# Kernel optimization log

Hardware: AMD Instinct MI355X
Metric: run time of the kernel (lower is better)

Reference implementation:

```python
import jax, jax.numpy as jnp
import numpy as np
import math

B, N, C_IN, C_OUT, K, RATIO = 16, 4096, 256, 512, 16, 0.25
N_OUT = math.ceil(N * RATIO)  # 1024
BN_EPS = 1e-5


def fps_indices(p, n):
    """Farthest point sampling. p: [B,N,3] -> local indices [B,n] (deterministic start at 0, eval mode)."""
    def fps_one(pts):  # [N,3]
        d0 = jnp.sum((pts - pts[0]) ** 2, axis=-1)          # [N]
        idxs0 = jnp.zeros((n,), jnp.int32)                  # idx[0] = 0
        def body(i, st):
            d, idxs = st
            nxt = jnp.argmax(d).astype(jnp.int32)
            idxs = idxs.at[i].set(nxt)
            d = jnp.minimum(d, jnp.sum((pts - pts[nxt]) ** 2, axis=-1))
            return (d, idxs)
        _, idxs = jax.lax.fori_loop(1, n, body, (d0, idxs0))
        return idxs
    return jax.vmap(fps_one)(p)


def setup_inputs() -> dict:
    key = jax.random.key(0)
    ks = jax.random.split(key, 6)
    x = jax.random.normal(ks[0], (B, N, C_IN), jnp.float32)
    p = jax.random.normal(ks[1], (B, N, 3), jnp.float32)
    sid_euc = jax.random.randint(ks[2], (B * N, K), 0, B * N).astype(jnp.int64)
    tid_euc = jax.random.randint(ks[3], (B * N, K), 0, B * N).astype(jnp.int64)
    W = jax.random.normal(ks[4], (C_OUT, C_IN), jnp.float32) * (1.0 / np.sqrt(C_IN))
    b = jax.random.normal(ks[5], (C_OUT,), jnp.float32) * 0.02
    gamma = jnp.ones((C_OUT,), jnp.float32)
    beta = jnp.zeros((C_OUT,), jnp.float32)
    run_mean = jnp.zeros((C_OUT,), jnp.float32)
    run_var = jnp.ones((C_OUT,), jnp.float32)
    return {"x": x, "p": p, "sid_euc": sid_euc, "tid_euc": tid_euc,
            "W": W, "b": b, "gamma": gamma, "beta": beta,
            "run_mean": run_mean, "run_var": run_var}


def reference(x, p, sid_euc, tid_euc, W, b, gamma, beta, run_mean, run_var):
    Bsz, Npts, _ = x.shape
    n = N_OUT
    Kn = sid_euc.shape[1]
    # MLP: pointwise Linear + BatchNorm (eval) + ReLU
    h = jnp.einsum('bnc,oc->bno', x, W) + b                       # [B,N,C_OUT]
    h = (h - run_mean) * (gamma / jnp.sqrt(run_var + BN_EPS)) + beta
    h = jax.nn.relu(h)
    # FPS -> global flat indices into B*N
    fid_local = fps_indices(p, n)                                  # [B,n]
    fid = (fid_local + jnp.arange(Bsz, dtype=jnp.int32)[:, None] * Npts).reshape(-1)
    # sample coords
    p_flat = p.reshape(Bsz * Npts, -1)
    p_out = p_flat[fid].reshape(Bsz, n, -1)                        # [B,n,3]
    # gather K neighbors of each sampled point, max-pool over K
    sid = sid_euc[fid].reshape(-1)                                 # [B*n*K]
    h_flat = h.reshape(Bsz * Npts, -1)
    x_out = h_flat[sid].reshape(Bsz, n, Kn, -1).max(axis=-2)       # [B,n,C_OUT]
    return (x_out, p_out)
```

## Files before the change

### kernel.cpp

```cpp
#include <hip/hip_runtime.h>
#include <hip/hip_bf16.h>

#define BATCH   16
#define NPTS    4096
#define CIN     256
#define COUT    512
#define KNN     16
#define NOUT    1024
#define XOUT_ELEMS 8388608
#define LDA     40

typedef __attribute__((ext_vector_type(4))) float f32x4;
typedef __attribute__((ext_vector_type(8))) short bf16x8;

__device__ __forceinline__ unsigned short f2bf_rne(float f) {
    unsigned u = __float_as_uint(f);
    return (unsigned short)((u + 0x7FFFu + ((u >> 16) & 1u)) >> 16);
}
__device__ __forceinline__ float bf2f(unsigned short s) {
    return __uint_as_float(((unsigned)s) << 16);
}

__device__ __forceinline__ float wave_max_dpp(float v) {
    int x, y;
    x = __float_as_int(v);
    y = __builtin_amdgcn_update_dpp(x, x, 0x111, 0xf, 0xf, false);
    v = fmaxf(v, __int_as_float(y)); x = __float_as_int(v);
    y = __builtin_amdgcn_update_dpp(x, x, 0x112, 0xf, 0xf, false);
    v = fmaxf(v, __int_as_float(y)); x = __float_as_int(v);
    y = __builtin_amdgcn_update_dpp(x, x, 0x114, 0xf, 0xf, false);
    v = fmaxf(v, __int_as_float(y)); x = __float_as_int(v);
    y = __builtin_amdgcn_update_dpp(x, x, 0x118, 0xf, 0xf, false);
    v = fmaxf(v, __int_as_float(y)); x = __float_as_int(v);
    y = __builtin_amdgcn_update_dpp(x, x, 0x142, 0xf, 0xf, false);
    v = fmaxf(v, __int_as_float(y)); x = __float_as_int(v);
    y = __builtin_amdgcn_update_dpp(x, x, 0x143, 0xf, 0xf, false);
    v = fmaxf(v, __int_as_float(y));
    return v;
}

extern "C" __global__ void __launch_bounds__(256)
fused_fps_gemm(const float* __restrict__ x, const float* __restrict__ p,
               const float* __restrict__ W, const float* __restrict__ bias,
               const float* __restrict__ gamma, const float* __restrict__ beta,
               const float* __restrict__ rmean, const float* __restrict__ rvar,
               int* __restrict__ fid, unsigned short* __restrict__ h)
{
    extern __shared__ char smem[];
    const int t = threadIdx.x;

    if (blockIdx.x < BATCH) {
        const int b = blockIdx.x;
        float* lx = (float*)smem;
        float* ly = lx + NPTS;
        float* lz = ly + NPTS;
        unsigned long long* warr = (unsigned long long*)(lz + NPTS);

        const float* pb = p + (size_t)b * NPTS * 3;
        for (int l = t; l < NPTS * 3; l += 256) {
            float v = pb[l];
            int pi = l / 3;
            int c = l - pi * 3;
            if (c == 0) lx[pi] = v; else if (c == 1) ly[pi] = v; else lz[pi] = v;
        }
        __syncthreads();

        float px[16], py[16], pz[16], d[16];
        const int base = t << 4;
#pragma unroll
        for (int j = 0; j < 16; ++j) {
            px[j] = lx[base + j]; py[j] = ly[base + j]; pz[j] = lz[base + j];
            d[j] = 3.4028235e38f;
        }
        if (t == 0) fid[b * NOUT] = b * NPTS;

        int winner = 0;
        for (int i = 1; i < NOUT; ++i) {
            float wx = lx[winner], wy = ly[winner], wz = lz[winner];
            float bestd = -1.0f;
            int   bestj = 0;
#pragma unroll
            for (int j = 0; j < 16; ++j) {
                float dx = __fsub_rn(px[j], wx);
                float dy = __fsub_rn(py[j], wy);
                float dz = __fsub_rn(pz[j], wz);
                float s  = __fadd_rn(__fadd_rn(__fmul_rn(dx, dx), __fmul_rn(dy, dy)),
                                     __fmul_rn(dz, dz));
                float nd = fminf(d[j], s);
                d[j] = nd;
                bool gt = nd > bestd;
                bestd = gt ? nd : bestd;
                bestj = gt ? j  : bestj;
            }
            float vmax = wave_max_dpp(bestd);
            float wmax = __int_as_float(
                __builtin_amdgcn_readlane(__float_as_int(vmax), 63));
            unsigned long long msk = __ballot(bestd == wmax);
            int lead = (int)__builtin_ctzll(msk);
            int wbpi = __builtin_amdgcn_readlane(base + bestj, lead);
            unsigned long long key = ((unsigned long long)__float_as_uint(wmax) << 32)
                                   | (unsigned)(NPTS - 1 - wbpi);
            unsigned long long* wrow = warr + ((i & 1) << 2);
            if ((t & 63) == 0) wrow[t >> 6] = key;
            __syncthreads();
            unsigned long long k0 = wrow[0], k1 = wrow[1], k2 = wrow[2], k3 = wrow[3];
            if (k1 > k0) k0 = k1;
            if (k3 > k2) k2 = k3;
            if (k2 > k0) k0 = k2;
            winner = NPTS - 1 - (int)(unsigned)(k0 & 0xffffffffull);
            if (t == 0) fid[b * NOUT + i] = b * NPTS + winner;
        }
    } else {
        const int bid = blockIdx.x - BATCH;
        const int bm = bid >> 2;
        const int bn = bid & 3;
        short* As = (short*)smem;
        short* Bs = As + 128 * LDA;

        const int lane = t & 63;
        const int wv = t >> 6;
        const int wm = wv >> 1, wn = wv & 1;
        const int quad = lane >> 4, l16 = lane & 15;
        const int m0 = bm * 128, n0 = bn * 128;

        f32x4 acc[4][4];
        const f32x4 zero = {0.0f, 0.0f, 0.0f, 0.0f};
#pragma unroll
        for (int a = 0; a < 4; ++a)
#pragma unroll
            for (int bb = 0; bb < 4; ++bb) acc[a][bb] = zero;

        const int srow = t >> 3;
        const int scol = (t & 7) << 2;

        for (int ks = 0; ks < 8; ++ks) {
            const int k0 = ks * 32;
            __syncthreads();
#pragma unroll
            for (int it = 0; it < 4; ++it) {
                int row = srow + it * 32;
                float4 va = *(const float4*)(x + (size_t)(m0 + row) * CIN + k0 + scol);
                short4 pa = make_short4((short)f2bf_rne(va.x), (short)f2bf_rne(va.y),
                                        (short)f2bf_rne(va.z), (short)f2bf_rne(va.w));
                *(short4*)(As + row * LDA + scol) = pa;
                float4 vb = *(const float4*)(W + (size_t)(n0 + row) * CIN + k0 + scol);
                short4 pb2 = make_short4((short)f2bf_rne(vb.x), (short)f2bf_rne(vb.y),
                                         (short)f2bf_rne(vb.z), (short)f2bf_rne(vb.w));
                *(short4*)(Bs + row * LDA + scol) = pb2;
            }
            __syncthreads();
            bf16x8 af[4], bfr[4];
#pragma unroll
            for (int tm = 0; tm < 4; ++tm)
                af[tm] = *(const bf16x8*)(As + (wm * 64 + tm * 16 + l16) * LDA + quad * 8);
#pragma unroll
            for (int tn = 0; tn < 4; ++tn)
                bfr[tn] = *(const bf16x8*)(Bs + (wn * 64 + tn * 16 + l16) * LDA + quad * 8);
#pragma unroll
            for (int tm = 0; tm < 4; ++tm)
#pragma unroll
                for (int tn = 0; tn < 4; ++tn)
                    acc[tm][tn] = __builtin_amdgcn_mfma_f32_16x16x32_bf16(
                        af[tm], bfr[tn], acc[tm][tn], 0, 0, 0);
        }
#pragma unroll
        for (int tn = 0; tn < 4; ++tn) {
            int c = n0 + wn * 64 + tn * 16 + l16;
            float sc = gamma[c] / sqrtf(rvar[c] + 1e-5f);
            float sh = (bias[c] - rmean[c]) * sc + beta[c];
#pragma unroll
            for (int tm = 0; tm < 4; ++tm) {
                int rbase = m0 + wm * 64 + tm * 16 + quad * 4;
#pragma unroll
                for (int r = 0; r < 4; ++r) {
                    float v = fmaxf(acc[tm][tn][r] * sc + sh, 0.0f);
                    h[(size_t)(rbase + r) * COUT + c] = f2bf_rne(v);
                }
            }
        }
    }
}

extern "C" __global__ void __launch_bounds__(128)
gather_maxpool(const int* __restrict__ sid32, const float* __restrict__ p,
               const int* __restrict__ fid, const unsigned short* __restrict__ h,
               float* __restrict__ out)
{
    const int j = blockIdx.x;
    const int t = threadIdx.x;
    __shared__ int rows[KNN];
    const int frow = fid[j];
    bool is64 = (sid32[1] == 0) && (sid32[3] == 0) && (sid32[5] == 0);
    if (t < KNN) {
        long long e = (long long)frow * KNN + t;
        rows[t] = is64 ? sid32[e * 2] : sid32[e];
    }
    if (t < 3) out[(size_t)XOUT_ELEMS + (size_t)j * 3 + t] = p[(size_t)frow * 3 + t];
    __syncthreads();

    const int c4 = t << 2;
    float m0 = -3.4028235e38f, m1 = m0, m2 = m0, m3 = m0;
#pragma unroll
    for (int k = 0; k < KNN; ++k) {
        const ushort4 v = *(const ushort4*)(h + (size_t)rows[k] * COUT + c4);
        m0 = fmaxf(m0, bf2f(v.x));
        m1 = fmaxf(m1, bf2f(v.y));
        m2 = fmaxf(m2, bf2f(v.z));
        m3 = fmaxf(m3, bf2f(v.w));
    }
    *(float4*)(out + (size_t)j * COUT + c4) = make_float4(m0, m1, m2, m3);
}

extern "C" void kernel_launch(void* const* d_in, const int* in_sizes, int n_in,
                              void* d_out, int out_size, void* d_ws, size_t ws_size,
                              hipStream_t stream)
{
    const float* x     = (const float*)d_in[0];
    const float* p     = (const float*)d_in[1];
    const int*   sid   = (const int*)d_in[2];
    const float* W     = (const float*)d_in[4];
    const float* bias  = (const float*)d_in[5];
    const float* gamma = (const float*)d_in[6];
    const float* beta  = (const float*)d_in[7];
    const float* rmean = (const float*)d_in[8];
    const float* rvar  = (const float*)d_in[9];
    float* out = (float*)d_out;

    int* fid = (int*)d_ws;
    unsigned short* h = (unsigned short*)((char*)d_ws + 65536);

    const size_t lds = 3 * NPTS * 4 + 2 * 4 * 8;
    hipLaunchKernelGGL(fused_fps_gemm, dim3(BATCH + 512 * 4), dim3(256), lds, stream,
                       x, p, W, bias, gamma, beta, rmean, rvar, fid, h);
    hipLaunchKernelGGL(gather_maxpool, dim3(BATCH * NOUT), dim3(128), 0, stream,
                       sid, p, fid, h, out);
}
```

Measured before the change: 745.7 us.

## Fuse gather-maxpool into persistent kernel with flag-based FPS streaming

Merges the gather/maxpool stage into the FPS+GEMM kernel. Gather blocks spin on a GEMM completion counter and on per-sample fid entries, which are pre-filled with -1 by a memset, so gathering can overlap the serial FPS loop instead of waiting for a second launch. The FPS blocks now write sampled coordinates directly, and the inner distance loop uses packed float2 math. The cost is spin-waiting gather blocks that hold CU slots, two extra memsets, and a risk of deadlock or ordering problems if the FPS blocks are not scheduled ahead of the waiting blocks.

```diff
diff --git a/kernel.cpp b/kernel.cpp
--- a/kernel.cpp
+++ b/kernel.cpp
@@ -9,8 +9,11 @@
 #define NOUT    1024
 #define XOUT_ELEMS 8388608
 #define LDA     40
+#define GEMM_BLOCKS 2048
+#define GATHER_BLOCKS 8192
 
 typedef __attribute__((ext_vector_type(4))) float f32x4;
+typedef __attribute__((ext_vector_type(2))) float f32x2;
 typedef __attribute__((ext_vector_type(8))) short bf16x8;
 
 __device__ __forceinline__ unsigned short f2bf_rne(float f) {
@@ -40,21 +43,25 @@
 }
 
 extern "C" __global__ void __launch_bounds__(256)
-fused_fps_gemm(const float* __restrict__ x, const float* __restrict__ p,
-               const float* __restrict__ W, const float* __restrict__ bias,
-               const float* __restrict__ gamma, const float* __restrict__ beta,
-               const float* __restrict__ rmean, const float* __restrict__ rvar,
-               int* __restrict__ fid, unsigned short* __restrict__ h)
+fused_all(const float* __restrict__ x, const float* __restrict__ p,
+          const int* __restrict__ sid32, const float* __restrict__ W,
+          const float* __restrict__ bias, const float* __restrict__ gamma,
+          const float* __restrict__ beta, const float* __restrict__ rmean,
+          const float* __restrict__ rvar, int* __restrict__ fid,
+          unsigned* __restrict__ cnt, unsigned short* __restrict__ h,
+          float* __restrict__ out)
 {
     extern __shared__ char smem[];
     const int t = threadIdx.x;
 
     if (blockIdx.x < BATCH) {
+#pragma clang fp contract(off)
         const int b = blockIdx.x;
         float* lx = (float*)smem;
         float* ly = lx + NPTS;
         float* lz = ly + NPTS;
         unsigned long long* warr = (unsigned long long*)(lz + NPTS);
+        float* pout = out + XOUT_ELEMS + (size_t)b * NOUT * 3;
 
         const float* pb = p + (size_t)b * NPTS * 3;
         for (int l = t; l < NPTS * 3; l += 256) {
@@ -65,32 +72,45 @@
         }
         __syncthreads();
 
-        float px[16], py[16], pz[16], d[16];
+        f32x2 px2[8], py2[8], pz2[8], d2[8];
         const int base = t << 4;
 #pragma unroll
-        for (int j = 0; j < 16; ++j) {
-            px[j] = lx[base + j]; py[j] = ly[base + j]; pz[j] = lz[base + j];
-            d[j] = 3.4028235e38f;
-        }
-        if (t == 0) fid[b * NOUT] = b * NPTS;
+        for (int j = 0; j < 8; ++j) {
+            px2[j] = *(const f32x2*)(lx + base + (j << 1));
+            py2[j] = *(const f32x2*)(ly + base + (j << 1));
+            pz2[j] = *(const f32x2*)(lz + base + (j << 1));
+            d2[j]  = (f32x2){3.4028235e38f, 3.4028235e38f};
+        }
+        if (t == 0)
+            __hip_atomic_store(&fid[b * NOUT], b * NPTS, __ATOMIC_RELAXED,
+                               __HIP_MEMORY_SCOPE_AGENT);
 
         int winner = 0;
         for (int i = 1; i < NOUT; ++i) {
             float wx = lx[winner], wy = ly[winner], wz = lz[winner];
+            if (t == 0) {
+                float* po = pout + (size_t)(i - 1) * 3;
+                po[0] = wx; po[1] = wy; po[2] = wz;
+            }
+            f32x2 wx2 = {wx, wx}, wy2 = {wy, wy}, wz2 = {wz, wz};
             float bestd = -1.0f;
             int   bestj = 0;
 #pragma unroll
-            for (int j = 0; j < 16; ++j) {
-                float dx = __fsub_rn(px[j], wx);
-                float dy = __fsub_rn(py[j], wy);
-                float dz = __fsub_rn(pz[j], wz);
-                float s  = __fadd_rn(__fadd_rn(__fmul_rn(dx, dx), __fmul_rn(dy, dy)),
-                                     __fmul_rn(dz, dz));
-                float nd = fminf(d[j], s);
-                d[j] = nd;
-                bool gt = nd > bestd;
-                bestd = gt ? nd : bestd;
-                bestj = gt ? j  : bestj;
+            for (int j = 0; j < 8; ++j) {
+                f32x2 dx = px2[j] - wx2;
+                f32x2 dy = py2[j] - wy2;
+                f32x2 dz = pz2[j] - wz2;
+                f32x2 s  = ((dx * dx) + (dy * dy)) + (dz * dz);
+                f32x2 nd;
+                nd.x = fminf(d2[j].x, s.x);
+                nd.y = fminf(d2[j].y, s.y);
+                d2[j] = nd;
+                bool g0 = nd.x > bestd;
+                bestd = g0 ? nd.x : bestd;
+                bestj = g0 ? (j << 1) : bestj;
+                bool g1 = nd.y > bestd;
+                bestd = g1 ? nd.y : bestd;
+                bestj = g1 ? (j << 1) + 1 : bestj;
             }
             float vmax = wave_max_dpp(bestd);
             float wmax = __int_as_float(
@@ -108,9 +128,15 @@
             if (k3 > k2) k2 = k3;
             if (k2 > k0) k0 = k2;
             winner = NPTS - 1 - (int)(unsigned)(k0 & 0xffffffffull);
-            if (t == 0) fid[b * NOUT + i] = b * NPTS + winner;
-        }
-    } else {
+            if (t == 0)
+                __hip_atomic_store(&fid[b * NOUT + i], b * NPTS + winner,
+                                   __ATOMIC_RELAXED, __HIP_MEMORY_SCOPE_AGENT);
+        }
+        if (t == 0) {
+            float* po = pout + (size_t)(NOUT - 1) * 3;
+            po[0] = lx[winner]; po[1] = ly[winner]; po[2] = lz[winner];
+        }
+    } else if (blockIdx.x < BATCH + GEMM_BLOCKS) {
         const int bid = blockIdx.x - BATCH;
         const int bm = bid >> 2;
         const int bn = bid & 3;
@@ -178,37 +204,61 @@
                 }
             }
         }
+        __threadfence();
+        __syncthreads();
+        if (t == 0)
+            __hip_atomic_fetch_add(cnt, 1u, __ATOMIC_RELEASE,
+                                   __HIP_MEMORY_SCOPE_AGENT);
+    } else {
+        const int gb = blockIdx.x - (BATCH + GEMM_BLOCKS);
+        const int j0 = gb << 1;
+        int* rows  = (int*)smem;
+        int* frows = rows + 32;
+        const int g = t >> 7, tl = t & 127;
+
+        if (tl == 0) {
+            if (g == 0) {
+                long guard = 0;
+                unsigned c;
+                do {
+                    c = __hip_atomic_load(cnt, __ATOMIC_ACQUIRE,
+                                          __HIP_MEMORY_SCOPE_AGENT);
+                    if (c >= (unsigned)GEMM_BLOCKS) break;
+                    __builtin_amdgcn_s_sleep(32);
+                } while (++guard < (1 << 21));
+            }
+            long guard = 0;
+            int v;
+            do {
+                v = __hip_atomic_load(&fid[j0 + g], __ATOMIC_RELAXED,
+                                      __HIP_MEMORY_SCOPE_AGENT);
+                if (v >= 0) break;
+                __builtin_amdgcn_s_sleep(16);
+            } while (++guard < (1 << 21));
+            frows[g] = v;
+            __threadfence();
+        }
+        __syncthreads();
+        const int frow = frows[g];
+        bool is64 = (sid32[1] == 0) && (sid32[3] == 0) && (sid32[5] == 0);
+        if (tl < KNN) {
+            long long e = (long long)frow * KNN + tl;
+            rows[g * KNN + tl] = is64 ? sid32[e * 2] : sid32[e];
+        }
+        __syncthreads();
+
+        const int c4 = tl << 2;
+        float m0 = -3.4028235e38f, m1 = m0, m2 = m0, m3 = m0;
+#pragma unroll
+        for (int k = 0; k < KNN; ++k) {
+            const ushort4 v = *(const ushort4*)(h + (size_t)rows[g * KNN + k] * COUT + c4);
+            m0 = fmaxf(m0, bf2f(v.x));
+            m1 = fmaxf(m1, bf2f(v.y));
+            m2 = fmaxf(m2, bf2f(v.z));
+            m3 = fmaxf(m3, bf2f(v.w));
+        }
+        *(float4*)(out + (size_t)(j0 + g) * COUT + c4) = make_float4(m0, m1, m2, m3);
     }
-}
-
-extern "C" __global__ void __launch_bounds__(128)
-gather_maxpool(const int* __restrict__ sid32, const float* __restrict__ p,
-               const int* __restrict__ fid, const unsigned short* __restrict__ h,
-               float* __restrict__ out)
-{
-    const int j = blockIdx.x;
-    const int t = threadIdx.x;
-    __shared__ int rows[KNN];
-    const int frow = fid[j];
-    bool is64 = (sid32[1] == 0) && (sid32[3] == 0) && (sid32[5] == 0);
-    if (t < KNN) {
-        long long e = (long long)frow * KNN + t;
-        rows[t] = is64 ? sid32[e * 2] : sid32[e];
-    }
-    if (t < 3) out[(size_t)XOUT_ELEMS + (size_t)j * 3 + t] = p[(size_t)frow * 3 + t];
-    __syncthreads();
-
-    const int c4 = t << 2;
-    float m0 = -3.4028235e38f, m1 = m0, m2 = m0, m3 = m0;
-#pragma unroll
-    for (int k = 0; k < KNN; ++k) {
-        const ushort4 v = *(const ushort4*)(h + (size_t)rows[k] * COUT + c4);
-        m0 = fmaxf(m0, bf2f(v.x));
-        m1 = fmaxf(m1, bf2f(v.y));
-        m2 = fmaxf(m2, bf2f(v.z));
-        m3 = fmaxf(m3, bf2f(v.w));
-    }
-    *(float4*)(out + (size_t)j * COUT + c4) = make_float4(m0, m1, m2, m3);
 }
 
 extern "C" void kernel_launch(void* const* d_in, const int* in_sizes, int n_in,
@@ -226,12 +276,16 @@
     const float* rvar  = (const float*)d_in[9];
     float* out = (float*)d_out;
 
-    int* fid = (int*)d_ws;
-    unsigned short* h = (unsigned short*)((char*)d_ws + 65536);
+    int*      fid = (int*)d_ws;
+    unsigned* cnt = (unsigned*)((char*)d_ws + 65536);
+    unsigned short* h = (unsigned short*)((char*)d_ws + 65792);
+
+    hipMemsetAsync(d_ws, 0xFF, 65536, stream);
+    hipMemsetAsync((char*)d_ws + 65536, 0, 4, stream);
 
     const size_t lds = 3 * NPTS * 4 + 2 * 4 * 8;
-    hipLaunchKernelGGL(fused_fps_gemm, dim3(BATCH + 512 * 4), dim3(256), lds, stream,
-                       x, p, W, bias, gamma, beta, rmean, rvar, fid, h);
-    hipLaunchKernelGGL(gather_maxpool, dim3(BATCH * NOUT), dim3(128), 0, stream,
-                       sid, p, fid, h, out);
-}
+    hipLaunchKernelGGL(fused_all, dim3(BATCH + GEMM_BLOCKS + GATHER_BLOCKS),
+                       dim3(256), lds, stream,
+                       x, p, sid, W, bias, gamma, beta, rmean, rvar,
+                       fid, cnt, h, out);
+}
```

Result: slower. 1.207 ms (+61.9%).

## Widen FPS blocks to 1024 threads and restructure GEMM blocks into dual groups

Applied to the files above, without the earlier changes.

The FPS blocks now use 1024 threads, each owning 4 points instead of 16. This shortens the serial per-iteration distance/argmax work, and the 16 wave keys are reduced with a 64-bit DPP max across lanes. FPS also writes the sampled coordinates directly, so the gather kernel no longer has to. The GEMM blocks become 1024-thread blocks split into two independent 512-thread groups, each computing two 128x128 tiles in sequence. The block-wide syncs are shared by both groups, and the larger block size may lower occupancy.

```diff
diff --git a/kernel.cpp b/kernel.cpp
--- a/kernel.cpp
+++ b/kernel.cpp
@@ -9,8 +9,10 @@
 #define NOUT    1024
 #define XOUT_ELEMS 8388608
 #define LDA     40
+#define DYN_LDS 49408
 
 typedef __attribute__((ext_vector_type(4))) float f32x4;
+typedef __attribute__((ext_vector_type(2))) float f32x2;
 typedef __attribute__((ext_vector_type(8))) short bf16x8;
 
 __device__ __forceinline__ unsigned short f2bf_rne(float f) {
@@ -39,25 +41,41 @@
     return v;
 }
 
-extern "C" __global__ void __launch_bounds__(256)
-fused_fps_gemm(const float* __restrict__ x, const float* __restrict__ p,
-               const float* __restrict__ W, const float* __restrict__ bias,
-               const float* __restrict__ gamma, const float* __restrict__ beta,
-               const float* __restrict__ rmean, const float* __restrict__ rvar,
-               int* __restrict__ fid, unsigned short* __restrict__ h)
+template <int CTRL>
+__device__ __forceinline__ void dpp_u64_max_step(unsigned& klo, unsigned& khi) {
+    unsigned olo = (unsigned)__builtin_amdgcn_update_dpp(
+        (int)klo, (int)klo, CTRL, 0xf, 0xf, false);
+    unsigned ohi = (unsigned)__builtin_amdgcn_update_dpp(
+        (int)khi, (int)khi, CTRL, 0xf, 0xf, false);
+    bool take = (ohi > khi) || (ohi == khi && olo > klo);
+    klo = take ? olo : klo;
+    khi = take ? ohi : khi;
+}
+
+extern "C" __global__ void __launch_bounds__(1024)
+fps_gemm(const float* __restrict__ x, const float* __restrict__ p,
+         const float* __restrict__ W, const float* __restrict__ bias,
+         const float* __restrict__ gamma, const float* __restrict__ beta,
+         const float* __restrict__ rmean, const float* __restrict__ rvar,
+         int* __restrict__ fid, unsigned short* __restrict__ h,
+         float* __restrict__ out)
 {
     extern __shared__ char smem[];
     const int t = threadIdx.x;
+    const int lane = t & 63;
+    const int wv = t >> 6;
 
     if (blockIdx.x < BATCH) {
+#pragma clang fp contract(off)
         const int b = blockIdx.x;
         float* lx = (float*)smem;
         float* ly = lx + NPTS;
         float* lz = ly + NPTS;
         unsigned long long* warr = (unsigned long long*)(lz + NPTS);
+        float* pout = out + XOUT_ELEMS + (size_t)b * NOUT * 3;
 
         const float* pb = p + (size_t)b * NPTS * 3;
-        for (int l = t; l < NPTS * 3; l += 256) {
+        for (int l = t; l < NPTS * 3; l += 1024) {
             float v = pb[l];
             int pi = l / 3;
             int c = l - pi * 3;
@@ -65,32 +83,43 @@
         }
         __syncthreads();
 
-        float px[16], py[16], pz[16], d[16];
-        const int base = t << 4;
-#pragma unroll
-        for (int j = 0; j < 16; ++j) {
-            px[j] = lx[base + j]; py[j] = ly[base + j]; pz[j] = lz[base + j];
-            d[j] = 3.4028235e38f;
+        f32x2 px2[2], py2[2], pz2[2], d2[2];
+        const int base = t << 2;
+#pragma unroll
+        for (int j = 0; j < 2; ++j) {
+            px2[j] = *(const f32x2*)(lx + base + (j << 1));
+            py2[j] = *(const f32x2*)(ly + base + (j << 1));
+            pz2[j] = *(const f32x2*)(lz + base + (j << 1));
+            d2[j]  = (f32x2){3.4028235e38f, 3.4028235e38f};
         }
         if (t == 0) fid[b * NOUT] = b * NPTS;
 
         int winner = 0;
         for (int i = 1; i < NOUT; ++i) {
             float wx = lx[winner], wy = ly[winner], wz = lz[winner];
+            if (t == 0) {
+                float* po = pout + (size_t)(i - 1) * 3;
+                po[0] = wx; po[1] = wy; po[2] = wz;
+            }
+            f32x2 wx2 = {wx, wx}, wy2 = {wy, wy}, wz2 = {wz, wz};
             float bestd = -1.0f;
             int   bestj = 0;
 #pragma unroll
-            for (int j = 0; j < 16; ++j) {
-                float dx = __fsub_rn(px[j], wx);
-                float dy = __fsub_rn(py[j], wy);
-                float dz = __fsub_rn(pz[j], wz);
-                float s  = __fadd_rn(__fadd_rn(__fmul_rn(dx, dx), __fmul_rn(dy, dy)),
-                                     __fmul_rn(dz, dz));
-                float nd = fminf(d[j], s);
-                d[j] = nd;
-                bool gt = nd > bestd;
-                bestd = gt ? nd : bestd;
-                bestj = gt ? j  : bestj;
+            for (int j = 0; j < 2; ++j) {
+                f32x2 dx = px2[j] - wx2;
+                f32x2 dy = py2[j] - wy2;
+                f32x2 dz = pz2[j] - wz2;
+                f32x2 s  = ((dx * dx) + (dy * dy)) + (dz * dz);
+                f32x2 nd;
+                nd.x = fminf(d2[j].x, s.x);
+                nd.y = fminf(d2[j].y, s.y);
+                d2[j] = nd;
+                bool g0 = nd.x > bestd;
+                bestd = g0 ? nd.x : bestd;
+                bestj = g0 ? (j << 1) : bestj;
+                bool g1 = nd.y > bestd;
+                bestd = g1 ? nd.y : bestd;
+                bestj = g1 ? (j << 1) + 1 : bestj;
             }
             float vmax = wave_max_dpp(bestd);
             float wmax = __int_as_float(
@@ -100,91 +129,102 @@
             int wbpi = __builtin_amdgcn_readlane(base + bestj, lead);
             unsigned long long key = ((unsigned long long)__float_as_uint(wmax) << 32)
                                    | (unsigned)(NPTS - 1 - wbpi);
-            unsigned long long* wrow = warr + ((i & 1) << 2);
-            if ((t & 63) == 0) wrow[t >> 6] = key;
+            unsigned long long* wrow = warr + ((i & 1) << 4);
+            if (lane == 0) wrow[wv] = key;
             __syncthreads();
-            unsigned long long k0 = wrow[0], k1 = wrow[1], k2 = wrow[2], k3 = wrow[3];
-            if (k1 > k0) k0 = k1;
-            if (k3 > k2) k2 = k3;
-            if (k2 > k0) k0 = k2;
-            winner = NPTS - 1 - (int)(unsigned)(k0 & 0xffffffffull);
+            unsigned long long kk = wrow[lane & 15];
+            unsigned klo = (unsigned)kk, khi = (unsigned)(kk >> 32);
+            dpp_u64_max_step<0x111>(klo, khi);
+            dpp_u64_max_step<0x112>(klo, khi);
+            dpp_u64_max_step<0x114>(klo, khi);
+            dpp_u64_max_step<0x118>(klo, khi);
+            unsigned wlo = (unsigned)__builtin_amdgcn_readlane((int)klo, 15);
+            winner = NPTS - 1 - (int)wlo;
             if (t == 0) fid[b * NOUT + i] = b * NPTS + winner;
+        }
+        if (t == 0) {
+            float* po = pout + (size_t)(NOUT - 1) * 3;
+            po[0] = lx[winner]; po[1] = ly[winner]; po[2] = lz[winner];
         }
     } else {
         const int bid = blockIdx.x - BATCH;
-        const int bm = bid >> 2;
-        const int bn = bid & 3;
-        short* As = (short*)smem;
+        const int g  = t >> 9;
+        const int ts = t & 511;
+        short* As = (short*)(smem + g * 20480);
         short* Bs = As + 128 * LDA;
 
-        const int lane = t & 63;
-        const int wv = t >> 6;
-        const int wm = wv >> 1, wn = wv & 1;
-        const int quad = lane >> 4, l16 = lane & 15;
-        const int m0 = bm * 128, n0 = bn * 128;
-
-        f32x4 acc[4][4];
-        const f32x4 zero = {0.0f, 0.0f, 0.0f, 0.0f};
-#pragma unroll
-        for (int a = 0; a < 4; ++a)
-#pragma unroll
-            for (int bb = 0; bb < 4; ++bb) acc[a][bb] = zero;
-
-        const int srow = t >> 3;
-        const int scol = (t & 7) << 2;
-
-        for (int ks = 0; ks < 8; ++ks) {
-            const int k0 = ks * 32;
+        const int sl  = ts & 63;
+        const int swv = ts >> 6;
+        const int wm = swv >> 1;
+        const int wn = swv & 1;
+        const int quad = sl >> 4, l16 = sl & 15;
+        const int srow = ts >> 3;
+        const int scol = (ts & 7) << 2;
+
+        for (int half = 0; half < 2; ++half) {
+            const int tt = (bid * 2 + g) * 2 + half;
+            const int m0 = (tt >> 2) * 128, n0 = (tt & 3) * 128;
+
+            f32x4 acc[2][4];
+            const f32x4 zero = {0.0f, 0.0f, 0.0f, 0.0f};
+#pragma unroll
+            for (int a = 0; a < 2; ++a)
+#pragma unroll
+                for (int bb = 0; bb < 4; ++bb) acc[a][bb] = zero;
+
+            for (int ks = 0; ks < 8; ++ks) {
+                const int k0 = ks * 32;
+                __syncthreads();
+#pragma unroll
+                for (int it = 0; it < 2; ++it) {
+                    int row = srow + it * 64;
+                    float4 va = *(const float4*)(x + (size_t)(m0 + row) * CIN + k0 + scol);
+                    short4 pa = make_short4((short)f2bf_rne(va.x), (short)f2bf_rne(va.y),
+                                            (short)f2bf_rne(va.z), (short)f2bf_rne(va.w));
+                    *(short4*)(As + row * LDA + scol) = pa;
+                    float4 vb = *(const float4*)(W + (size_t)(n0 + row) * CIN + k0 + scol);
+                    short4 pb2 = make_short4((short)f2bf_rne(vb.x), (short)f2bf_rne(vb.y),
+                                             (short)f2bf_rne(vb.z), (short)f2bf_rne(vb.w));
+                    *(short4*)(Bs + row * LDA + scol) = pb2;
+                }
+                __syncthreads();
+                bf16x8 af[2], bfr[4];
+#pragma unroll
+                for (int tm = 0; tm < 2; ++tm)
+                    af[tm] = *(const bf16x8*)(As + (wm * 32 + tm * 16 + l16) * LDA + quad * 8);
+#pragma unroll
+                for (int tn = 0; tn < 4; ++tn)
+                    bfr[tn] = *(const bf16x8*)(Bs + (wn * 64 + tn * 16 + l16) * LDA + quad * 8);
+#pragma unroll
+                for (int tm = 0; tm < 2; ++tm)
+#pragma unroll
+                    for (int tn = 0; tn < 4; ++tn)
+                        acc[tm][tn] = __builtin_amdgcn_mfma_f32_16x16x32_bf16(
+                            af[tm], bfr[tn], acc[tm][tn], 0, 0, 0);
+            }
+#pragma unroll
+            for (int tn = 0; tn < 4; ++tn) {
+                int c = n0 + wn * 64 + tn * 16 + l16;
+                float sc = gamma[c] / sqrtf(rvar[c] + 1e-5f);
+                float sh = (bias[c] - rmean[c]) * sc + beta[c];
+#pragma unroll
+                for (int tm = 0; tm < 2; ++tm) {
+                    int rbase = m0 + wm * 32 + tm * 16 + quad * 4;
+#pragma unroll
+                    for (int r = 0; r < 4; ++r) {
+                        float v = fmaxf(acc[tm][tn][r] * sc + sh, 0.0f);
+                        h[(size_t)(rbase + r) * COUT + c] = f2bf_rne(v);
+                    }
+                }
+            }
             __syncthreads();
-#pragma unroll
-            for (int it = 0; it < 4; ++it) {
-                int row = srow + it * 32;
-                float4 va = *(const float4*)(x + (size_t)(m0 + row) * CIN + k0 + scol);
-                short4 pa = make_short4((short)f2bf_rne(va.x), (short)f2bf_rne(va.y),
-                                        (short)f2bf_rne(va.z), (short)f2bf_rne(va.w));
-                *(short4*)(As + row * LDA + scol) = pa;
-                float4 vb = *(const float4*)(W + (size_t)(n0 + row) * CIN + k0 + scol);
-                short4 pb2 = make_short4((short)f2bf_rne(vb.x), (short)f2bf_rne(vb.y),
-                                         (short)f2bf_rne(vb.z), (short)f2bf_rne(vb.w));
-                *(short4*)(Bs + row * LDA + scol) = pb2;
-            }
-            __syncthreads();
-            bf16x8 af[4], bfr[4];
-#pragma unroll
-            for (int tm = 0; tm < 4; ++tm)
-                af[tm] = *(const bf16x8*)(As + (wm * 64 + tm * 16 + l16) * LDA + quad * 8);
-#pragma unroll
-            for (int tn = 0; tn < 4; ++tn)
-                bfr[tn] = *(const bf16x8*)(Bs + (wn * 64 + tn * 16 + l16) * LDA + quad * 8);
-#pragma unroll
-            for (int tm = 0; tm < 4; ++tm)
-#pragma unroll
-                for (int tn = 0; tn < 4; ++tn)
-                    acc[tm][tn] = __builtin_amdgcn_mfma_f32_16x16x32_bf16(
-                        af[tm], bfr[tn], acc[tm][tn], 0, 0, 0);
-        }
-#pragma unroll
-        for (int tn = 0; tn < 4; ++tn) {
-            int c = n0 + wn * 64 + tn * 16 + l16;
-            float sc = gamma[c] / sqrtf(rvar[c] + 1e-5f);
-            float sh = (bias[c] - rmean[c]) * sc + beta[c];
-#pragma unroll
-            for (int tm = 0; tm < 4; ++tm) {
-                int rbase = m0 + wm * 64 + tm * 16 + quad * 4;
-#pragma unroll
-                for (int r = 0; r < 4; ++r) {
-                    float v = fmaxf(acc[tm][tn][r] * sc + sh, 0.0f);
-                    h[(size_t)(rbase + r) * COUT + c] = f2bf_rne(v);
-                }
-            }
         }
     }
 }
 
 extern "C" __global__ void __launch_bounds__(128)
-gather_maxpool(const int* __restrict__ sid32, const float* __restrict__ p,
-               const int* __restrict__ fid, const unsigned short* __restrict__ h,
-               float* __restrict__ out)
+gather_maxpool(const int* __restrict__ sid32, const int* __restrict__ fid,
+               const unsigned short* __restrict__ h, float* __restrict__ out)
 {
     const int j = blockIdx.x;
     const int t = threadIdx.x;
@@ -195,7 +235,6 @@
         long long e = (long long)frow * KNN + t;
         rows[t] = is64 ? sid32[e * 2] : sid32[e];
     }
-    if (t < 3) out[(size_t)XOUT_ELEMS + (size_t)j * 3 + t] = p[(size_t)frow * 3 + t];
     __syncthreads();
 
     const int c4 = t << 2;
@@ -227,11 +266,10 @@
     float* out = (float*)d_out;
 
     int* fid = (int*)d_ws;
-    unsigned short* h = (unsigned short*)((char*)d_ws + 65536);
-
-    const size_t lds = 3 * NPTS * 4 + 2 * 4 * 8;
-    hipLaunchKernelGGL(fused_fps_gemm, dim3(BATCH + 512 * 4), dim3(256), lds, stream,
-                       x, p, W, bias, gamma, beta, rmean, rvar, fid, h);
+    unsigned short* h = (unsigned short*)((char*)d_ws + 65792);
+
+    hipLaunchKernelGGL(fps_gemm, dim3(BATCH + 512), dim3(1024), DYN_LDS, stream,
+                       x, p, W, bias, gamma, beta, rmean, rvar, fid, h, out);
     hipLaunchKernelGGL(gather_maxpool, dim3(BATCH * NOUT), dim3(128), 0, stream,
-                       sid, p, fid, h, out);
-}
+                       sid, fid, h, out);
+}
```

New measurement: 1.006 ms. 1.35x slower.

## Replace FPS per-iteration barrier with tagged LDS spin-wait and packed float2 math

Applied to the files above, without the earlier changes.

Each FPS iteration no longer uses __syncthreads to combine the four per-wave maxima. Waves publish tagged keys with workgroup-scope atomic release stores and spin on acquire loads until all four tags match. The distance update is written with float2 vectors, presumably to allow packed FP32 instructions, with fp contraction disabled to keep rounding identical. The sampled coordinates are now written directly by the FPS block, which removes that gather from the maxpool kernel. The spin-wait costs busy polling of LDS and has a guard-based escape, and the tag scheme relies on double-buffered slots staying consistent.

```diff
diff --git a/kernel.cpp b/kernel.cpp
--- a/kernel.cpp
+++ b/kernel.cpp
@@ -9,9 +9,12 @@
 #define NOUT    1024
 #define XOUT_ELEMS 8388608
 #define LDA     40
+#define DYN_LDS 49408
 
 typedef __attribute__((ext_vector_type(4))) float f32x4;
+typedef __attribute__((ext_vector_type(2))) float f32x2;
 typedef __attribute__((ext_vector_type(8))) short bf16x8;
+typedef unsigned long long u64;
 
 __device__ __forceinline__ unsigned short f2bf_rne(float f) {
     unsigned u = __float_as_uint(f);
@@ -40,21 +43,26 @@
 }
 
 extern "C" __global__ void __launch_bounds__(256)
-fused_fps_gemm(const float* __restrict__ x, const float* __restrict__ p,
-               const float* __restrict__ W, const float* __restrict__ bias,
-               const float* __restrict__ gamma, const float* __restrict__ beta,
-               const float* __restrict__ rmean, const float* __restrict__ rvar,
-               int* __restrict__ fid, unsigned short* __restrict__ h)
+fps_gemm(const float* __restrict__ x, const float* __restrict__ p,
+         const float* __restrict__ W, const float* __restrict__ bias,
+         const float* __restrict__ gamma, const float* __restrict__ beta,
+         const float* __restrict__ rmean, const float* __restrict__ rvar,
+         int* __restrict__ fid, unsigned short* __restrict__ h,
+         float* __restrict__ out)
 {
     extern __shared__ char smem[];
     const int t = threadIdx.x;
+    const int lane = t & 63;
+    const int wv = t >> 6;
 
     if (blockIdx.x < BATCH) {
+#pragma clang fp contract(off)
         const int b = blockIdx.x;
         float* lx = (float*)smem;
         float* ly = lx + NPTS;
         float* lz = ly + NPTS;
-        unsigned long long* warr = (unsigned long long*)(lz + NPTS);
+        u64* keys = (u64*)(lz + NPTS);
+        float* pout = out + XOUT_ELEMS + (size_t)b * NOUT * 3;
 
         const float* pb = p + (size_t)b * NPTS * 3;
         for (int l = t; l < NPTS * 3; l += 256) {
@@ -63,52 +71,90 @@
             int c = l - pi * 3;
             if (c == 0) lx[pi] = v; else if (c == 1) ly[pi] = v; else lz[pi] = v;
         }
+        if (t < 4) {
+            keys[4 + t] = (u64)(0u << 12);
+            keys[t]     = (u64)(1u << 12);
+        }
         __syncthreads();
 
-        float px[16], py[16], pz[16], d[16];
+        f32x2 px2[8], py2[8], pz2[8], d2[8];
         const int base = t << 4;
 #pragma unroll
-        for (int j = 0; j < 16; ++j) {
-            px[j] = lx[base + j]; py[j] = ly[base + j]; pz[j] = lz[base + j];
-            d[j] = 3.4028235e38f;
+        for (int j = 0; j < 8; ++j) {
+            px2[j] = *(const f32x2*)(lx + base + (j << 1));
+            py2[j] = *(const f32x2*)(ly + base + (j << 1));
+            pz2[j] = *(const f32x2*)(lz + base + (j << 1));
+            d2[j]  = (f32x2){3.4028235e38f, 3.4028235e38f};
         }
         if (t == 0) fid[b * NOUT] = b * NPTS;
 
         int winner = 0;
         for (int i = 1; i < NOUT; ++i) {
             float wx = lx[winner], wy = ly[winner], wz = lz[winner];
+            if (t == 0) {
+                float* po = pout + (size_t)(i - 1) * 3;
+                po[0] = wx; po[1] = wy; po[2] = wz;
+            }
+            f32x2 wx2 = {wx, wx}, wy2 = {wy, wy}, wz2 = {wz, wz};
             float bestd = -1.0f;
             int   bestj = 0;
 #pragma unroll
-            for (int j = 0; j < 16; ++j) {
-                float dx = __fsub_rn(px[j], wx);
-                float dy = __fsub_rn(py[j], wy);
-                float dz = __fsub_rn(pz[j], wz);
-                float s  = __fadd_rn(__fadd_rn(__fmul_rn(dx, dx), __fmul_rn(dy, dy)),
-                                     __fmul_rn(dz, dz));
-                float nd = fminf(d[j], s);
-                d[j] = nd;
-                bool gt = nd > bestd;
-                bestd = gt ? nd : bestd;
-                bestj = gt ? j  : bestj;
+            for (int j = 0; j < 8; ++j) {
+                f32x2 dx = px2[j] - wx2;
+                f32x2 dy = py2[j] - wy2;
+                f32x2 dz = pz2[j] - wz2;
+                f32x2 s  = ((dx * dx) + (dy * dy)) + (dz * dz);
+                f32x2 nd;
+                nd.x = fminf(d2[j].x, s.x);
+                nd.y = fminf(d2[j].y, s.y);
+                d2[j] = nd;
+                bool g0 = nd.x > bestd;
+                bestd = g0 ? nd.x : bestd;
+                bestj = g0 ? (j << 1) : bestj;
+                bool g1 = nd.y > bestd;
+                bestd = g1 ? nd.y : bestd;
+                bestj = g1 ? (j << 1) + 1 : bestj;
             }
             float vmax = wave_max_dpp(bestd);
             float wmax = __int_as_float(
                 __builtin_amdgcn_readlane(__float_as_int(vmax), 63));
-            unsigned long long msk = __ballot(bestd == wmax);
+            u64 msk = __ballot(bestd == wmax);
             int lead = (int)__builtin_ctzll(msk);
             int wbpi = __builtin_amdgcn_readlane(base + bestj, lead);
-            unsigned long long key = ((unsigned long long)__float_as_uint(wmax) << 32)
-                                   | (unsigned)(NPTS - 1 - wbpi);
-            unsigned long long* wrow = warr + ((i & 1) << 2);
-            if ((t & 63) == 0) wrow[t >> 6] = key;
-            __syncthreads();
-            unsigned long long k0 = wrow[0], k1 = wrow[1], k2 = wrow[2], k3 = wrow[3];
+            const unsigned tag = (unsigned)i & 1023u;
+            u64 key = ((u64)__float_as_uint(wmax) << 32)
+                    | (tag << 12) | (unsigned)(NPTS - 1 - wbpi);
+            u64* slot = keys + ((i & 1) << 2);
+            if (lane == 0)
+                __hip_atomic_store(&slot[wv], key, __ATOMIC_RELEASE,
+                                   __HIP_MEMORY_SCOPE_WORKGROUP);
+            u64 k0, k1, k2, k3;
+            int guard = 0;
+            for (;;) {
+                k0 = __hip_atomic_load(&slot[0], __ATOMIC_ACQUIRE,
+                                       __HIP_MEMORY_SCOPE_WORKGROUP);
+                k1 = __hip_atomic_load(&slot[1], __ATOMIC_ACQUIRE,
+                                       __HIP_MEMORY_SCOPE_WORKGROUP);
+                k2 = __hip_atomic_load(&slot[2], __ATOMIC_ACQUIRE,
+                                       __HIP_MEMORY_SCOPE_WORKGROUP);
+                k3 = __hip_atomic_load(&slot[3], __ATOMIC_ACQUIRE,
+                                       __HIP_MEMORY_SCOPE_WORKGROUP);
+                unsigned t0 = ((unsigned)k0 >> 12) & 1023u;
+                unsigned t1 = ((unsigned)k1 >> 12) & 1023u;
+                unsigned t2 = ((unsigned)k2 >> 12) & 1023u;
+                unsigned t3 = ((unsigned)k3 >> 12) & 1023u;
+                if ((t0 == tag) & (t1 == tag) & (t2 == tag) & (t3 == tag)) break;
+                if (++guard > (1 << 22)) break;
+            }
             if (k1 > k0) k0 = k1;
             if (k3 > k2) k2 = k3;
             if (k2 > k0) k0 = k2;
-            winner = NPTS - 1 - (int)(unsigned)(k0 & 0xffffffffull);
+            winner = NPTS - 1 - (int)(k0 & 0xFFFu);
             if (t == 0) fid[b * NOUT + i] = b * NPTS + winner;
+        }
+        if (t == 0) {
+            float* po = pout + (size_t)(NOUT - 1) * 3;
+            po[0] = lx[winner]; po[1] = ly[winner]; po[2] = lz[winner];
         }
     } else {
         const int bid = blockIdx.x - BATCH;
@@ -117,8 +163,6 @@
         short* As = (short*)smem;
         short* Bs = As + 128 * LDA;
 
-        const int lane = t & 63;
-        const int wv = t >> 6;
         const int wm = wv >> 1, wn = wv & 1;
         const int quad = lane >> 4, l16 = lane & 15;
         const int m0 = bm * 128, n0 = bn * 128;
@@ -182,9 +226,8 @@
 }
 
 extern "C" __global__ void __launch_bounds__(128)
-gather_maxpool(const int* __restrict__ sid32, const float* __restrict__ p,
-               const int* __restrict__ fid, const unsigned short* __restrict__ h,
-               float* __restrict__ out)
+gather_maxpool(const int* __restrict__ sid32, const int* __restrict__ fid,
+               const unsigned short* __restrict__ h, float* __restrict__ out)
 {
     const int j = blockIdx.x;
     const int t = threadIdx.x;
@@ -195,7 +238,6 @@
         long long e = (long long)frow * KNN + t;
         rows[t] = is64 ? sid32[e * 2] : sid32[e];
     }
-    if (t < 3) out[(size_t)XOUT_ELEMS + (size_t)j * 3 + t] = p[(size_t)frow * 3 + t];
     __syncthreads();
 
     const int c4 = t << 2;
@@ -227,11 +269,10 @@
     float* out = (float*)d_out;
 
     int* fid = (int*)d_ws;
-    unsigned short* h = (unsigned short*)((char*)d_ws + 65536);
-
-    const size_t lds = 3 * NPTS * 4 + 2 * 4 * 8;
-    hipLaunchKernelGGL(fused_fps_gemm, dim3(BATCH + 512 * 4), dim3(256), lds, stream,
-                       x, p, W, bias, gamma, beta, rmean, rvar, fid, h);
+    unsigned short* h = (unsigned short*)((char*)d_ws + 65792);
+
+    hipLaunchKernelGGL(fps_gemm, dim3(BATCH + 2048), dim3(256), DYN_LDS, stream,
+                       x, p, W, bias, gamma, beta, rmean, rvar, fid, h, out);
     hipLaunchKernelGGL(gather_maxpool, dim3(BATCH * NOUT), dim3(128), 0, stream,
-                       sid, p, fid, h, out);
-}
+                       sid, fid, h, out);
+}
```

Measured after the change: 958.2 us. 1.29x slower.
